# Kernel tuning notes

Measured on AMD Instinct MI355X. Metric: run time of the kernel, lower is better.

The kernel has to match this reference:

```python
import jax, jax.numpy as jnp
import numpy as np

B, N, C_IN, C_OUT, K = 16, 4096, 3, 64, 20
EPS = 1e-5


def setup_inputs() -> dict:
    key = jax.random.key(0)
    ks = jax.random.split(key, 6)
    x = jax.random.normal(ks[0], (B * N, C_IN), dtype=jnp.float32)
    batch = jnp.repeat(jnp.arange(B, dtype=jnp.int32), N)
    # MLP([2*C_IN, C_OUT, C_OUT]) per PyG: Linear -> BatchNorm -> ReLU -> Linear (plain last)
    w1 = jax.random.normal(ks[1], (2 * C_IN, C_OUT), dtype=jnp.float32) / np.sqrt(2 * C_IN)
    b1 = jnp.zeros((C_OUT,), dtype=jnp.float32)
    gamma = jnp.ones((C_OUT,), dtype=jnp.float32)
    beta = jnp.zeros((C_OUT,), dtype=jnp.float32)
    w2 = jax.random.normal(ks[2], (C_OUT, C_OUT), dtype=jnp.float32) / np.sqrt(C_OUT)
    b2 = jnp.zeros((C_OUT,), dtype=jnp.float32)
    return {"x": x, "batch": batch, "w1": w1, "b1": b1,
            "gamma": gamma, "beta": beta, "w2": w2, "b2": b2}


def reference(x, batch, w1, b1, gamma, beta, w2, b2):
    # batch is sorted with equal-size clouds -> reshape to [B, N, C]
    xb = x.reshape(B, N, C_IN)
    # pairwise squared distances within each cloud: [B, N, N]
    sq = jnp.sum(xb * xb, axis=-1)
    d = sq[:, :, None] + sq[:, None, :] - 2.0 * jnp.einsum('bnc,bmc->bnm', xb, xb)
    # k nearest neighbors (self included, matching PyG knn): [B, N, K]
    idx = jax.lax.top_k(-d, K)[1]
    # gather neighbor features: [B, N, K, C]
    xj = jax.vmap(lambda pts, ind: pts[ind])(xb, idx)
    xi = xb[:, :, None, :]
    # edge features [x_i, x_j - x_i]: [B, N, K, 2C]
    e = jnp.concatenate([jnp.broadcast_to(xi, (B, N, K, C_IN)), xj - xi], axis=-1)
    # MLP: Linear -> BatchNorm(train mode) -> ReLU -> Linear
    h = e @ w1 + b1  # [B, N, K, C_OUT]
    mean = jnp.mean(h, axis=(0, 1, 2))
    var = jnp.var(h, axis=(0, 1, 2))
    h = (h - mean) * jax.lax.rsqrt(var + EPS) * gamma + beta
    h = jax.nn.relu(h)
    h = h @ w2 + b2
    # max aggregation over neighbors -> [B*N, C_OUT]
    return jnp.max(h, axis=2).reshape(B * N, C_OUT)
```

## Files before the change

kernel.cpp:

```cpp
#include <hip/hip_runtime.h>
#include <math.h>
#include <float.h>

#define B_   16
#define N_   4096
#define CIN  3
#define COUT 64
#define KNN  20
#define EPS_ 1e-5


__device__ __forceinline__ unsigned expand10(unsigned v) {
    v = (v | (v << 16)) & 0x030000FFu;
    v = (v | (v << 8))  & 0x0300F00Fu;
    v = (v | (v << 4))  & 0x030C30C3u;
    v = (v | (v << 2))  & 0x09249249u;
    return v;
}
__device__ __forceinline__ unsigned quant10(float v) {
    int q = (int)((v + 4.0f) * 128.0f);
    return (unsigned)min(1023, max(0, q));
}

__global__ __launch_bounds__(1024) void morton_bucket_kernel(
    const float* __restrict__ x, int* __restrict__ perm,
    double* __restrict__ stats)
{
    __shared__ int hist[1024];
    __shared__ int scanbuf[1024];
    __shared__ int offs[1024];
    const int b = blockIdx.x, tid = threadIdx.x;
    const float* xb = x + (size_t)b * N_ * CIN;

    if (b == 0 && tid < 27) stats[tid] = 0.0;

    hist[tid] = 0;
    __syncthreads();

    int keys[4];
#pragma unroll
    for (int i = 0; i < 4; ++i) {
        int p = tid + i * 1024;
        float v0 = xb[p * 3 + 0], v1 = xb[p * 3 + 1], v2 = xb[p * 3 + 2];
        unsigned m = (expand10(quant10(v0)) << 2) |
                     (expand10(quant10(v1)) << 1) |
                      expand10(quant10(v2));
        keys[i] = (int)(m >> 20);
        atomicAdd(&hist[keys[i]], 1);
    }
    __syncthreads();

    int v = hist[tid];
    scanbuf[tid] = v;
    __syncthreads();
    for (int off = 1; off < 1024; off <<= 1) {
        int t = (tid >= off) ? scanbuf[tid - off] : 0;
        __syncthreads();
        scanbuf[tid] += t;
        __syncthreads();
    }
    offs[tid] = scanbuf[tid] - v;
    __syncthreads();

#pragma unroll
    for (int i = 0; i < 4; ++i) {
        int p = tid + i * 1024;
        int pos = atomicAdd(&offs[keys[i]], 1);
        perm[b * N_ + pos] = p;
    }
}

__global__ __launch_bounds__(512) void knn_f64_kernel(
    const float* __restrict__ x, const int* __restrict__ perm,
    int* __restrict__ idx_out, double* __restrict__ stats)
{
    extern __shared__ __align__(16) char smem[];
    float4* pts = (float4*)smem;
    unsigned short* j16 = (unsigned short*)(smem + 65536);
    double* scr = (double*)smem;

    const int b    = blockIdx.y;
    const int tid  = threadIdx.x;
    const int wave = tid >> 6;
    const int lane = tid & 63;
    const int r    = wave >> 2;
    const int q    = wave & 3;
    const float* xb = x + (size_t)b * N_ * CIN;

    for (int p = tid; p < N_; p += 512) {
        int j = perm[b * N_ + p];
        float v0 = xb[j * 3 + 0], v1 = xb[j * 3 + 1], v2 = xb[j * 3 + 2];
        float sq = __fadd_rn(__fadd_rn(__fmul_rn(v0, v0),
                                       __fmul_rn(v1, v1)),
                             __fmul_rn(v2, v2));
        pts[p] = make_float4(v0, v1, v2, sq);
        j16[p] = (unsigned short)j;
    }
    __syncthreads();

    const int rowg = blockIdx.x * 128 + r * 64;
    const float4 xf = pts[rowg + lane];
    const int jrow  = j16[rowg + lane];
    const float sqi = xf.w;

    auto mkd = [&](float4 p) -> float {
        float dot = __fadd_rn(__fadd_rn(__fmul_rn(xf.x, p.x),
                                        __fmul_rn(xf.y, p.y)),
                              __fmul_rn(xf.z, p.z));
        return __fsub_rn(__fadd_rn(sqi, p.w), __fmul_rn(2.0f, dot));
    };
    auto sortable = [&](float d) -> unsigned {
        unsigned u = __float_as_uint(d);
        return u ^ (0x80000000u | (unsigned)((int)u >> 31));
    };

    double bk[KNN];
#pragma unroll
    for (int k = 0; k < KNN; ++k) bk[k] = 1e300;

    auto insert = [&](double key) {
        if (key < bk[KNN - 1]) {
            double m = key;
#pragma unroll
            for (int k = 0; k < KNN; ++k) {
                double old = bk[k];
                bk[k] = fmin(m, old);
                m     = fmax(old, m);
            }
        }
    };

    const int ta = rowg >> 2;
#pragma unroll
    for (int k = 0; k < KNN; ++k) {
        int p = 4 * ((ta + k) & 1023) + q;
        float4 a = pts[p];
        insert(fma((double)sortable(mkd(a)), 4096.0,
                   (double)(unsigned)j16[p]));
    }

    float d19f;
    {
        unsigned s19 = (unsigned)trunc(bk[KNN - 1] * (1.0 / 4096.0));
        unsigned u = (s19 >= 0x80000000u) ? (s19 ^ 0x80000000u) : ~s19;
        d19f = __uint_as_float(u);
    }

    for (int s = 0; s < 1024; s += 4) {
        int v0 = ((s + 0) * 509) & 1023;
        int v1 = ((s + 1) * 509) & 1023;
        int v2 = ((s + 2) * 509) & 1023;
        int v3 = ((s + 3) * 509) & 1023;
        int p0 = 4 * ((ta + v0) & 1023) + q;
        int p1 = 4 * ((ta + v1) & 1023) + q;
        int p2 = 4 * ((ta + v2) & 1023) + q;
        int p3 = 4 * ((ta + v3) & 1023) + q;
        float4 a0 = pts[p0];
        float4 a1 = pts[p1];
        float4 a2 = pts[p2];
        float4 a3 = pts[p3];
        float d0 = mkd(a0), d1 = mkd(a1), d2 = mkd(a2), d3 = mkd(a3);
        d0 = (v0 < 20) ? INFINITY : d0;
        d1 = (v1 < 20) ? INFINITY : d1;
        d2 = (v2 < 20) ? INFINITY : d2;
        d3 = (v3 < 20) ? INFINITY : d3;
        if ((d0 <= d19f) | (d1 <= d19f) | (d2 <= d19f) | (d3 <= d19f)) {
            unsigned j0 = j16[p0], j1 = j16[p1], j2 = j16[p2], j3 = j16[p3];
            insert(fma((double)sortable(d0), 4096.0, (double)j0));
            insert(fma((double)sortable(d1), 4096.0, (double)j1));
            insert(fma((double)sortable(d2), 4096.0, (double)j2));
            insert(fma((double)sortable(d3), 4096.0, (double)j3));
            unsigned s19 = (unsigned)trunc(bk[KNN - 1] * (1.0 / 4096.0));
            unsigned u = (s19 >= 0x80000000u) ? (s19 ^ 0x80000000u) : ~s19;
            d19f = __uint_as_float(u);
        }
    }
    __syncthreads();

    if (q & 1) {
        int base = ((r * 2 + (q >> 1)) * 64 + lane) * KNN;
#pragma unroll
        for (int k = 0; k < KNN; ++k) scr[base + k] = bk[k];
    }
    __syncthreads();
    if (!(q & 1)) {
        int base = ((r * 2 + (q >> 1)) * 64 + lane) * KNN;
#pragma unroll
        for (int k = 0; k < KNN; ++k) insert(scr[base + k]);
    }
    __syncthreads();
    if (q == 2) {
        int base = ((r * 2 + 1) * 64 + lane) * KNN;
#pragma unroll
        for (int k = 0; k < KNN; ++k) scr[base + k] = bk[k];
    }
    __syncthreads();
    if (q == 0) {
        int base = ((r * 2 + 1) * 64 + lane) * KNN;
#pragma unroll
        for (int k = 0; k < KNN; ++k) insert(scr[base + k]);

        const long long row = (long long)b * N_ + jrow;
        int bi[KNN];
#pragma unroll
        for (int k = 0; k < KNN; ++k) {
            double sp = trunc(bk[k] * (1.0 / 4096.0));
            bi[k] = (int)(bk[k] - sp * 4096.0);
        }
#pragma unroll
        for (int k = 0; k < KNN; ++k) idx_out[row * KNN + k] = bi[k];

        float acc[27];
#pragma unroll
        for (int t = 0; t < 27; ++t) acc[t] = 0.0f;
#pragma unroll
        for (int k = 0; k < KNN; ++k) {
            const float* pj = xb + bi[k] * 3;
            float e[6] = { xf.x, xf.y, xf.z,
                           pj[0] - xf.x, pj[1] - xf.y, pj[2] - xf.z };
            int t = 6;
#pragma unroll
            for (int a = 0; a < 6; ++a) {
                acc[a] += e[a];
#pragma unroll
                for (int bb = a; bb < 6; ++bb) acc[t++] += e[a] * e[bb];
            }
        }
#pragma unroll
        for (int t = 0; t < 27; ++t) {
            float v = acc[t];
            v += __shfl_down(v, 32); v += __shfl_down(v, 16);
            v += __shfl_down(v, 8);  v += __shfl_down(v, 4);
            v += __shfl_down(v, 2);  v += __shfl_down(v, 1);
            acc[t] = v;
        }
        if (lane == 0) {
#pragma unroll
            for (int t = 0; t < 27; ++t) atomicAdd(&stats[t], (double)acc[t]);
        }
    }
}

__global__ void bn_prep_kernel(
    const double* __restrict__ stats,
    const float* __restrict__ w1, const float* __restrict__ b1,
    const float* __restrict__ gamma, const float* __restrict__ beta,
    float* __restrict__ scale_shift)
{
    const int c = threadIdx.x;
    double s[6], S[6][6];
#pragma unroll
    for (int a = 0; a < 6; ++a) s[a] = stats[a];
    int t = 6;
#pragma unroll
    for (int a = 0; a < 6; ++a)
#pragma unroll
        for (int bb = a; bb < 6; ++bb) { S[a][bb] = stats[t]; S[bb][a] = stats[t]; ++t; }

    const double M = (double)B_ * N_ * KNN;
    double wc[6];
#pragma unroll
    for (int j = 0; j < 6; ++j) wc[j] = (double)w1[j * COUT + c];
    const double b1c = (double)b1[c];

    double sw = 0.0;
#pragma unroll
    for (int j = 0; j < 6; ++j) sw += s[j] * wc[j];
    double mean = sw / M + b1c;

    double qq = 0.0;
#pragma unroll
    for (int a = 0; a < 6; ++a)
#pragma unroll
        for (int bb = 0; bb < 6; ++bb) qq += S[a][bb] * wc[a] * wc[bb];
    double ex2 = (qq + 2.0 * b1c * sw) / M + b1c * b1c;
    double var = ex2 - mean * mean;

    double sc = (double)gamma[c] / sqrt(var + (double)EPS_);
    double sh = (double)beta[c] - mean * sc;
    scale_shift[c]        = (float)sc;
    scale_shift[COUT + c] = (float)sh;
}

typedef __attribute__((ext_vector_type(8))) short short8;
typedef __attribute__((ext_vector_type(4))) float f32x4;

__device__ __forceinline__ unsigned short f2bf_rn(float f) {
    unsigned u = __float_as_uint(f);
    unsigned lsb = (u >> 16) & 1u;
    return (unsigned short)((u + 0x7FFFu + lsb) >> 16);
}
__device__ __forceinline__ float bf2f(unsigned short h) {
    return __uint_as_float(((unsigned)h) << 16);
}

__global__ __launch_bounds__(256) void mlp_max_kernel(
    const float* __restrict__ x, const int* __restrict__ idx,
    const float* __restrict__ w1, const float* __restrict__ b1,
    const float* __restrict__ scale_shift,
    const float* __restrict__ w2, const float* __restrict__ b2,
    float* __restrict__ out)
{
    __shared__ __align__(16) unsigned short hbuf[4][16][136];
    __shared__ int idxs[4][320];
    __shared__ __align__(16) float4 sbuf[4][2][4][16];

    const int tid  = threadIdx.x;
    const int wv   = tid >> 6;
    const int lane = tid & 63;
    const int g    = lane >> 4;
    const int r15  = lane & 15;

    const int R     = (blockIdx.x * 4 + wv) * 16;
    const int bbase = (R >> 12) << 12;

    {
        const int* ip = idx + (size_t)R * KNN;
#pragma unroll
        for (int i = 0; i < 5; ++i)
            idxs[wv][lane + i * 64] = ip[lane + i * 64];
    }

    const int c  = lane;
    const float sc = scale_shift[c];
    const float sh = scale_shift[COUT + c];
    float w1p[6];
#pragma unroll
    for (int j = 0; j < 6; ++j) w1p[j] = w1[j * COUT + c] * sc;
    const float b1p = fmaf(b1[c], sc, sh);
    const float dw0 = w1p[0] - w1p[3];
    const float dw1 = w1p[1] - w1p[4];
    const float dw2 = w1p[2] - w1p[5];

    short8 Wh[2][4], Wl[2][4];
#pragma unroll
    for (int t = 0; t < 2; ++t)
#pragma unroll
        for (int n = 0; n < 4; ++n) {
            short8 hv, lv;
#pragma unroll
            for (int jj = 0; jj < 8; ++jj) {
                float w = w2[(t * 32 + g * 8 + jj) * COUT + n * 16 + r15];
                unsigned short hi = f2bf_rn(w);
                unsigned short lo = f2bf_rn(w - bf2f(hi));
                hv[jj] = (short)hi;
                lv[jj] = (short)lo;
            }
            Wh[t][n] = hv;
            Wl[t][n] = lv;
        }

    float base[16];
#pragma unroll
    for (int r = 0; r < 16; ++r) {
        const float* pi = x + (size_t)(R + r) * 3;
        float v = b1p;
        v = fmaf(pi[0], dw0, v);
        v = fmaf(pi[1], dw1, v);
        v = fmaf(pi[2], dw2, v);
        base[r] = v;
    }

    const int gr = lane >> 2;
    const int gk = lane & 3;
    auto gather_group = [&](int grp) {
        int kk = grp * 4 + gk;
        int j = idxs[wv][gr * KNN + kk];
        const float* pj = x + (size_t)(bbase + j) * 3;
        sbuf[wv][grp & 1][gk][gr] =
            make_float4(pj[0], pj[1], pj[2], 0.0f);
    };

    gather_group(0);

    f32x4 mx[4];
#pragma unroll
    for (int n = 0; n < 4; ++n) {
        mx[n][0] = -INFINITY; mx[n][1] = -INFINITY;
        mx[n][2] = -INFINITY; mx[n][3] = -INFINITY;
    }

    unsigned short* hb = &hbuf[wv][0][0];
    const unsigned short* rpnt = hb + r15 * 136;

    for (int grp = 0; grp < 5; ++grp) {
        if (grp + 1 < 5) gather_group(grp + 1);

#pragma unroll
        for (int kl = 0; kl < 4; ++kl) {
#pragma unroll
            for (int r = 0; r < 16; ++r) {
                float4 pv = sbuf[wv][grp & 1][kl][r];
                float h = base[r];
                h = fmaf(pv.x, w1p[3], h);
                h = fmaf(pv.y, w1p[4], h);
                h = fmaf(pv.z, w1p[5], h);
                h = fmaxf(h, 0.0f);
                hb[r * 136 + c] = f2bf_rn(h);
            }

            short8 Ah0 = *(const short8*)(rpnt + g * 8);
            short8 Ah1 = *(const short8*)(rpnt + 32 + g * 8);

            __builtin_amdgcn_s_setprio(1);
#pragma unroll
            for (int n = 0; n < 4; ++n) {
                f32x4 a = {0.0f, 0.0f, 0.0f, 0.0f};
                a = __builtin_amdgcn_mfma_f32_16x16x32_bf16(Ah0, Wh[0][n], a, 0, 0, 0);
                a = __builtin_amdgcn_mfma_f32_16x16x32_bf16(Ah1, Wh[1][n], a, 0, 0, 0);
                a = __builtin_amdgcn_mfma_f32_16x16x32_bf16(Ah0, Wl[0][n], a, 0, 0, 0);
                a = __builtin_amdgcn_mfma_f32_16x16x32_bf16(Ah1, Wl[1][n], a, 0, 0, 0);
                mx[n][0] = fmaxf(mx[n][0], a[0]);
                mx[n][1] = fmaxf(mx[n][1], a[1]);
                mx[n][2] = fmaxf(mx[n][2], a[2]);
                mx[n][3] = fmaxf(mx[n][3], a[3]);
            }
            __builtin_amdgcn_s_setprio(0);
        }
    }

    float b2v[4];
#pragma unroll
    for (int n = 0; n < 4; ++n) b2v[n] = b2[n * 16 + r15];
#pragma unroll
    for (int n = 0; n < 4; ++n)
#pragma unroll
        for (int rr = 0; rr < 4; ++rr)
            out[(size_t)(R + g * 4 + rr) * COUT + n * 16 + r15] =
                mx[n][rr] + b2v[n];
}

extern "C" void kernel_launch(void* const* d_in, const int* in_sizes, int n_in,
                              void* d_out, int out_size, void* d_ws, size_t ws_size,
                              hipStream_t stream)
{
    const float* x     = (const float*)d_in[0];
    const float* w1    = (const float*)d_in[2];
    const float* b1    = (const float*)d_in[3];
    const float* gamma = (const float*)d_in[4];
    const float* beta  = (const float*)d_in[5];
    const float* w2    = (const float*)d_in[6];
    const float* b2    = (const float*)d_in[7];
    float* out = (float*)d_out;

    char*   ws          = (char*)d_ws;
    double* stats       = (double*)ws;
    float*  scale_shift = (float*)(ws + 256);
    int*    idx         = (int*)(ws + 1024);
    int*    perm        = (int*)(ws + 1024 + (size_t)B_ * N_ * KNN * 4);

    static int _lds_once = []() {
        (void)hipFuncSetAttribute((const void*)knn_f64_kernel,
                                  hipFuncAttributeMaxDynamicSharedMemorySize,
                                  131072);
        return 0;
    }();
    (void)_lds_once;

    morton_bucket_kernel<<<B_, 1024, 0, stream>>>(x, perm, stats);
    knn_f64_kernel<<<dim3(32, 16), 512, 73728, stream>>>(x, perm, idx, stats);
    bn_prep_kernel<<<1, COUT, 0, stream>>>(stats, w1, b1, gamma, beta, scale_shift);
    mlp_max_kernel<<<(B_ * N_) / 64, 256, 0, stream>>>(x, idx, w1, b1, scale_shift,
                                                       w2, b2, out);
}
```

Measured before the change: 426.3 us.

## Split each KNN candidate scan across two waves with 1024-thread blocks

The KNN kernel now runs 1024 threads per block instead of 512. Each query row's candidate set is split across eight waves instead of four, using an extra half index h, so each wave scans 512 candidates instead of 1024. An added two-phase LDS merge combines the halves before the existing four-way merge. This is meant to shorten the serial per-thread scan and raise parallelism. In exchange it adds more synchronisation, merge work and register pressure under the larger launch bound.

```diff
diff --git a/kernel.cpp b/kernel.cpp
--- a/kernel.cpp
+++ b/kernel.cpp
@@ -70,7 +70,7 @@
     }
 }
 
-__global__ __launch_bounds__(512) void knn_f64_kernel(
+__global__ __launch_bounds__(1024) void knn_f64_kernel(
     const float* __restrict__ x, const int* __restrict__ perm,
     int* __restrict__ idx_out, double* __restrict__ stats)
 {
@@ -81,13 +81,14 @@
 
     const int b    = blockIdx.y;
     const int tid  = threadIdx.x;
-    const int wave = tid >> 6;
+    const int w    = tid >> 6;
     const int lane = tid & 63;
-    const int r    = wave >> 2;
-    const int q    = wave & 3;
+    const int r    = w >> 3;
+    const int q    = (w >> 1) & 3;
+    const int h    = w & 1;
     const float* xb = x + (size_t)b * N_ * CIN;
 
-    for (int p = tid; p < N_; p += 512) {
+    for (int p = tid; p < N_; p += 1024) {
         int j = perm[b * N_ + p];
         float v0 = xb[j * 3 + 0], v1 = xb[j * 3 + 1], v2 = xb[j * 3 + 2];
         float sq = __fadd_rn(__fadd_rn(__fmul_rn(v0, v0),
@@ -131,9 +132,12 @@
     };
 
     const int ta = rowg >> 2;
+    const int ua = ta >> 1;
+
 #pragma unroll
     for (int k = 0; k < KNN; ++k) {
-        int p = 4 * ((ta + k) & 1023) + q;
+        int u = (ua + k) & 511;
+        int p = 4 * (2 * u + h) + q;
         float4 a = pts[p];
         insert(fma((double)sortable(mkd(a)), 4096.0,
                    (double)(unsigned)j16[p]));
@@ -146,15 +150,15 @@
         d19f = __uint_as_float(u);
     }
 
-    for (int s = 0; s < 1024; s += 4) {
-        int v0 = ((s + 0) * 509) & 1023;
-        int v1 = ((s + 1) * 509) & 1023;
-        int v2 = ((s + 2) * 509) & 1023;
-        int v3 = ((s + 3) * 509) & 1023;
-        int p0 = 4 * ((ta + v0) & 1023) + q;
-        int p1 = 4 * ((ta + v1) & 1023) + q;
-        int p2 = 4 * ((ta + v2) & 1023) + q;
-        int p3 = 4 * ((ta + v3) & 1023) + q;
+    for (int s = 0; s < 512; s += 4) {
+        int v0 = ((s + 0) * 253) & 511;
+        int v1 = ((s + 1) * 253) & 511;
+        int v2 = ((s + 2) * 253) & 511;
+        int v3 = ((s + 3) * 253) & 511;
+        int p0 = 4 * (2 * ((ua + v0) & 511) + h) + q;
+        int p1 = 4 * (2 * ((ua + v1) & 511) + h) + q;
+        int p2 = 4 * (2 * ((ua + v2) & 511) + h) + q;
+        int p3 = 4 * (2 * ((ua + v3) & 511) + h) + q;
         float4 a0 = pts[p0];
         float4 a1 = pts[p1];
         float4 a2 = pts[p2];
@@ -177,25 +181,40 @@
     }
     __syncthreads();
 
-    if (q & 1) {
+    for (int ph = 0; ph < 2; ++ph) {
+        if (r == ph && h == 1) {
+            int base = (q * 64 + lane) * KNN;
+#pragma unroll
+            for (int k = 0; k < KNN; ++k) scr[base + k] = bk[k];
+        }
+        __syncthreads();
+        if (r == ph && h == 0) {
+            int base = (q * 64 + lane) * KNN;
+#pragma unroll
+            for (int k = 0; k < KNN; ++k) insert(scr[base + k]);
+        }
+        __syncthreads();
+    }
+
+    if (h == 0 && (q & 1)) {
         int base = ((r * 2 + (q >> 1)) * 64 + lane) * KNN;
 #pragma unroll
         for (int k = 0; k < KNN; ++k) scr[base + k] = bk[k];
     }
     __syncthreads();
-    if (!(q & 1)) {
+    if (h == 0 && !(q & 1)) {
         int base = ((r * 2 + (q >> 1)) * 64 + lane) * KNN;
 #pragma unroll
         for (int k = 0; k < KNN; ++k) insert(scr[base + k]);
     }
     __syncthreads();
-    if (q == 2) {
+    if (h == 0 && q == 2) {
         int base = ((r * 2 + 1) * 64 + lane) * KNN;
 #pragma unroll
         for (int k = 0; k < KNN; ++k) scr[base + k] = bk[k];
     }
     __syncthreads();
-    if (q == 0) {
+    if (h == 0 && q == 0) {
         int base = ((r * 2 + 1) * 64 + lane) * KNN;
 #pragma unroll
         for (int k = 0; k < KNN; ++k) insert(scr[base + k]);
@@ -458,7 +477,7 @@
     (void)_lds_once;
 
     morton_bucket_kernel<<<B_, 1024, 0, stream>>>(x, perm, stats);
-    knn_f64_kernel<<<dim3(32, 16), 512, 73728, stream>>>(x, perm, idx, stats);
+    knn_f64_kernel<<<dim3(32, 16), 1024, 73728, stream>>>(x, perm, idx, stats);
     bn_prep_kernel<<<1, COUT, 0, stream>>>(stats, w1, b1, gamma, beta, scale_shift);
     mlp_max_kernel<<<(B_ * N_) / 64, 256, 0, stream>>>(x, idx, w1, b1, scale_shift,
                                                        w2, b2, out);
```

Measured after the change: 545.3 us. +27.9%, slower.
